# Kernel optimization log

Measured on AMD Instinct MI355X. Metric: run time of the kernel, lower is better.

Reference implementation:

```python
import jax, jax.numpy as jnp
import numpy as np

# Uniform-scope sizes: B molecules, A atoms/mol, G fragments/mol, W map width,
# H hidden, L attention layers, S = G+1 (fg prompt row prepended per molecule)
B, A, G, W, H, L = 1024, 64, 31, 8, 512, 2
S = G + 1
DK = 32  # attention head dim (hard-coded in the module)


def _layernorm(x, g, b, eps):
    mu = jnp.mean(x, axis=-1, keepdims=True)
    var = jnp.var(x, axis=-1, keepdims=True)
    return g * (x - mu) * jax.lax.rsqrt(var + eps) + b


def setup_inputs() -> dict:
    key = jax.random.key(0)
    ks = jax.random.split(key, 16)
    s = 0.02
    return {
        "f_atom": jax.random.normal(ks[0], (B * A, H), jnp.float32),
        "f_group": jax.random.normal(ks[1], (B * G, H), jnp.float32),
        "fg": jax.random.normal(ks[2], (1, 3 * H), jnp.float32),
        "alpha": 0.1 * jnp.ones((1,), jnp.float32),
        "lr_w": jax.random.normal(ks[3], (3 * H, H), jnp.float32) * s,
        "lr_b": jnp.zeros((H,), jnp.float32),
        "wq_w": jax.random.normal(ks[4], (L, H, DK), jnp.float32) * s,
        "wq_b": jnp.zeros((L, DK), jnp.float32),
        "wk_w": jax.random.normal(ks[5], (L, H, DK), jnp.float32) * s,
        "wk_b": jnp.zeros((L, DK), jnp.float32),
        "wv_w": jax.random.normal(ks[6], (L, H, DK), jnp.float32) * s,
        "wv_b": jnp.zeros((L, DK), jnp.float32),
        "dense_w": jax.random.normal(ks[7], (L, DK, H), jnp.float32) * s,
        "dense_b": jnp.zeros((L, H), jnp.float32),
        "ln_g": jnp.ones((L, H), jnp.float32),
        "ln_b": jnp.zeros((L, H), jnp.float32),
        "lin_w": jax.random.normal(ks[8], (H, H), jnp.float32) * s,
        "lin_b": jnp.zeros((H,), jnp.float32),
        "norm_g": jnp.ones((H,), jnp.float32),
        "norm_b": jnp.zeros((H,), jnp.float32),
        "mapping": jax.random.randint(ks[9], (B * G, W), 0, A + 1, jnp.int64),
    }


def reference(f_atom, f_group, fg, alpha, lr_w, lr_b, wq_w, wq_b, wk_w, wk_b,
              wv_w, wv_b, dense_w, dense_b, ln_g, ln_b, lin_w, lin_b,
              norm_g, norm_b, mapping):
    # --- ragged gather + reduce + pad (vectorized: uniform scopes) ---
    a = f_atom.reshape(B, A, H)
    # prepend zero padding row per molecule (mapping index 0 -> zeros)
    a_pad = jnp.concatenate([jnp.zeros((B, 1, H), a.dtype), a], axis=1)  # [B,A+1,H]
    m = mapping.reshape(B, G, W)
    gathered = a_pad[jnp.arange(B)[:, None, None], m]  # [B,G,W,H]
    g = f_group.reshape(B, G, H)
    cur_g = jnp.concatenate(
        [gathered.sum(axis=2), gathered.max(axis=2), g], axis=-1)  # [B,G,3H]
    brics = jnp.concatenate(
        [jnp.broadcast_to(fg[None], (B, 1, 3 * H)), cur_g], axis=1)  # [B,S,3H]

    f_frag = jax.nn.relu(brics @ lr_w + lr_b)  # [B,S,H]

    # mask built from init_hiddens = f_frag (same for every layer)
    pm = (f_frag != 0).astype(f_frag.dtype)
    mask = jnp.einsum('bsh,bth->bst', pm, pm)  # [B,S,S]
    neg = jnp.asarray(-1e9, f_frag.dtype)
    scale = 1.0 / np.sqrt(DK)

    hs = f_frag
    attn = None
    for l in range(L):
        q = hs @ wq_w[l] + wq_b[l]
        k = hs @ wk_w[l] + wk_b[l]
        v = hs @ wv_w[l] + wv_b[l]
        scores = jnp.einsum('bsd,btd->bst', q, k) * scale
        scores = jnp.where(mask == 0, neg, scores)
        attn = jax.nn.softmax(scores, axis=-1)
        x = jnp.einsum('bst,btd->bsd', attn, v)
        dh = x @ dense_w[l] + dense_b[l]  # dropout is identity in eval
        hs = _layernorm(dh + hs, ln_g[l], ln_b[l], 1e-6)

    f_out = _layernorm(hs @ lin_w + lin_b, norm_g, norm_b, 1e-5) * alpha[0]
    return f_out[:, 0, :], attn
```

## Files before the change

### kernel.cpp

```cpp
#include <hip/hip_runtime.h>

#define B_   1024
#define A_   64
#define G_   31
#define W_   8
#define H_   512
#define L_   2
#define S_   32
#define DK_  32
#define K3H_ 1536

typedef short short8 __attribute__((ext_vector_type(8)));
typedef float floatx4 __attribute__((ext_vector_type(4)));

__device__ __forceinline__ float bf2f(unsigned short u){
  union { unsigned int i; float f; } x; x.i = ((unsigned int)u) << 16; return x.f;
}
__device__ __forceinline__ unsigned short f2bf(float f){
  union { float f; unsigned int i; } x; x.f = f;
  unsigned int u = x.i;
  return (unsigned short)((u + 0x7FFFu + ((u >> 16) & 1u)) >> 16);
}
__device__ __forceinline__ void gl_lds16(const unsigned short* g, unsigned short* l){
  __builtin_amdgcn_global_load_lds((const __attribute__((address_space(1))) unsigned int*)g,
                                   (__attribute__((address_space(3))) unsigned int*)l, 16, 0, 0);
}

__global__ __launch_bounds__(256) void prep_transpose(
    const float* __restrict__ lr_w, const float* __restrict__ lin_w,
    unsigned short* __restrict__ lr_wT, unsigned short* __restrict__ lin_wT){
  __shared__ float tile[64][65];
  int bx = blockIdx.x;
  const float* src; unsigned short* dst; int R, C;
  if (bx < 192){ src = lr_w;  dst = lr_wT;  R = 1536; C = 512; }
  else         { bx -= 192; src = lin_w; dst = lin_wT; R = 512;  C = 512; }
  int rt = bx >> 3, ct = bx & 7;
  int tid = threadIdx.x;
  int r16 = tid >> 4, c4 = tid & 15;
  #pragma unroll
  for (int p = 0; p < 4; ++p){
    int row = p*16 + r16;
    float4 v = *(const float4*)(src + (size_t)(rt*64 + row) * C + ct*64 + c4*4);
    tile[row][c4*4+0] = v.x; tile[row][c4*4+1] = v.y;
    tile[row][c4*4+2] = v.z; tile[row][c4*4+3] = v.w;
  }
  __syncthreads();
  int rr = tid >> 3, cc8 = tid & 7;
  #pragma unroll
  for (int p = 0; p < 2; ++p){
    int n = p*32 + rr;
    unsigned short o[8] __attribute__((aligned(16)));
    #pragma unroll
    for (int j = 0; j < 8; ++j) o[j] = f2bf(tile[cc8*8 + j][n]);
    *(uint4*)(dst + (size_t)(ct*64 + n) * R + rt*64 + cc8*8) = *(const uint4*)o;
  }
}

__global__ __launch_bounds__(256) void prep_small(
    const float* __restrict__ wq_w, const float* __restrict__ wk_w, const float* __restrict__ wv_w,
    const float* __restrict__ dense_w,
    unsigned short* __restrict__ qkvT, unsigned short* __restrict__ denseT){
  int i = blockIdx.x * 256 + threadIdx.x;
  if (i < 98304){
    int k = i & 511; int t = i >> 9; int n = t & 31; int u = t >> 5;
    int p = u % 3, l = u / 3;
    const float* src = (p == 0) ? wq_w : (p == 1) ? wk_w : wv_w;
    qkvT[((size_t)((l*3+p)*S_ + n)) * H_ + k] = f2bf(src[((size_t)(l*H_ + k)) * DK_ + n]);
    return;
  }
  i -= 98304;
  int k = i & 31; int t = i >> 5; int n = t & 511; int l = t >> 9;
  denseT[((size_t)(l*H_ + n)) * DK_ + k] = f2bf(dense_w[((size_t)(l*DK_ + k)) * H_ + n]);
}

__global__ __launch_bounds__(256) void build_brics(
    const float* __restrict__ f_atom, const float* __restrict__ f_group,
    const float* __restrict__ fg, const int* __restrict__ mapping,
    unsigned short* __restrict__ brics){
  int pair = blockIdx.x * 4 + (threadIdx.x >> 6);
  int b = pair >> 5, s = pair & 31;
  int t = threadIdx.x & 63;
  unsigned short* out = brics + (size_t)pair * K3H_;
  if (s == 0){
    for (int k = t; k < K3H_; k += 64) out[k] = f2bf(fg[k]);
    return;
  }
  int g = s - 1;
  const int* mp = mapping + ((size_t)(b * G_ + g)) * W_;
  int c0 = t * 8;
  float sum[8], mx[8];
  #pragma unroll
  for (int j = 0; j < 8; ++j){ sum[j] = 0.f; mx[j] = -3.4e38f; }
  for (int w = 0; w < W_; ++w){
    int idx = mp[w];
    if (idx == 0){
      #pragma unroll
      for (int j = 0; j < 8; ++j) mx[j] = fmaxf(mx[j], 0.f);
    } else {
      const float* row = f_atom + ((size_t)(b * A_ + idx - 1)) * H_ + c0;
      float4 v0 = *(const float4*)row;
      float4 v1 = *(const float4*)(row + 4);
      float v[8] = {v0.x,v0.y,v0.z,v0.w,v1.x,v1.y,v1.z,v1.w};
      #pragma unroll
      for (int j = 0; j < 8; ++j){ sum[j] += v[j]; mx[j] = fmaxf(mx[j], v[j]); }
    }
  }
  const float* grow = f_group + ((size_t)(b * G_ + g)) * H_ + c0;
  float4 g0 = *(const float4*)grow;
  float4 g1 = *(const float4*)(grow + 4);
  float gv[8] = {g0.x,g0.y,g0.z,g0.w,g1.x,g1.y,g1.z,g1.w};
  unsigned short tmp[8] __attribute__((aligned(16)));
  #pragma unroll
  for (int j = 0; j < 8; ++j) tmp[j] = f2bf(sum[j]);
  *(uint4*)(out + c0) = *(const uint4*)tmp;
  #pragma unroll
  for (int j = 0; j < 8; ++j) tmp[j] = f2bf(mx[j]);
  *(uint4*)(out + 512 + c0) = *(const uint4*)tmp;
  #pragma unroll
  for (int j = 0; j < 8; ++j) tmp[j] = f2bf(gv[j]);
  *(uint4*)(out + 1024 + c0) = *(const uint4*)tmp;
}

__global__ __launch_bounds__(256) void gemm_frag(
    const unsigned short* __restrict__ brics, const unsigned short* __restrict__ wT,
    const float* __restrict__ lr_b, unsigned short* __restrict__ f_frag){
  __shared__ __align__(16) unsigned short As[128*64];
  __shared__ __align__(16) unsigned short Bs[128*64];
  int tid = threadIdx.x;
  int bx = blockIdx.x;
  int xcd = bx & 7, slot = bx >> 3;
  int mtile = xcd + 8 * (slot >> 2);
  int ntile = slot & 3;
  int rowStart = mtile * 128, colStart = ntile * 128;
  int lane = tid & 63, wave = tid >> 6;
  int m16 = lane & 15, quad = lane >> 4;
  int wm = wave >> 1, wn = wave & 1;
  floatx4 acc[4][4];
  #pragma unroll
  for (int i = 0; i < 4; ++i)
    #pragma unroll
    for (int j = 0; j < 4; ++j) acc[i][j] = (floatx4){0.f,0.f,0.f,0.f};

  int srow = tid >> 3;
  int gchunk = (tid & 7) ^ (srow & 7);
  size_t aOff[4], bOff[4];
  #pragma unroll
  for (int p = 0; p < 4; ++p){
    aOff[p] = (size_t)(rowStart + p*32 + srow) * K3H_ + gchunk*8;
    bOff[p] = (size_t)(colStart + p*32 + srow) * K3H_ + gchunk*8;
  }
  int fsw0 = ((0*4 + quad) ^ (m16 & 7)) * 8;
  int fsw1 = ((1*4 + quad) ^ (m16 & 7)) * 8;

  for (int kt = 0; kt < K3H_/64; ++kt){
    int kbase = kt * 64;
    #pragma unroll
    for (int p = 0; p < 4; ++p){
      gl_lds16(brics + aOff[p] + kbase, As + p*2048 + (size_t)tid*8);
      gl_lds16(wT    + bOff[p] + kbase, Bs + p*2048 + (size_t)tid*8);
    }
    __syncthreads();
    #pragma unroll
    for (int ks = 0; ks < 2; ++ks){
      int fsw = ks ? fsw1 : fsw0;
      short8 af[4], bfr[4];
      #pragma unroll
      for (int i = 0; i < 4; ++i){
        af[i]  = *(const short8*)(As + (wm*64 + i*16 + m16)*64 + fsw);
        bfr[i] = *(const short8*)(Bs + (wn*64 + i*16 + m16)*64 + fsw);
      }
      #pragma unroll
      for (int i = 0; i < 4; ++i)
        #pragma unroll
        for (int j = 0; j < 4; ++j)
          acc[i][j] = __builtin_amdgcn_mfma_f32_16x16x32_bf16(af[i], bfr[j], acc[i][j], 0, 0, 0);
    }
    __syncthreads();
  }
  #pragma unroll
  for (int i = 0; i < 4; ++i)
    #pragma unroll
    for (int j = 0; j < 4; ++j){
      int col = colStart + wn*64 + j*16 + m16;
      float bias = lr_b[col];
      #pragma unroll
      for (int r = 0; r < 4; ++r){
        int row = rowStart + wm*64 + i*16 + quad*4 + r;
        float v = acc[i][j][r] + bias;
        v = v > 0.f ? v : 0.f;
        f_frag[(size_t)row * H_ + col] = f2bf(v);
      }
    }
}

__global__ __launch_bounds__(256) void attn_kernel(
    const unsigned short* __restrict__ f_frag,
    const unsigned short* __restrict__ qkvT, const unsigned short* __restrict__ denseT,
    const float* __restrict__ wq_b, const float* __restrict__ wk_b, const float* __restrict__ wv_b,
    const float* __restrict__ dense_b, const float* __restrict__ ln_g, const float* __restrict__ ln_b,
    unsigned short* __restrict__ hsf, float* __restrict__ out_attn){
  const int HP = 544, TP = 40;
  __shared__ __align__(16) unsigned short hs[S_*544];
  __shared__ __align__(16) unsigned short Qs[S_*40];
  __shared__ __align__(16) unsigned short Ks[S_*40];
  __shared__ __align__(16) unsigned short Vt[S_*40];
  __shared__ __align__(16) unsigned short Ps[S_*40];
  __shared__ __align__(16) unsigned short Xs[S_*40];
  __shared__ unsigned long long pmask[S_*8];
  __shared__ unsigned int mz[S_];
  int b = blockIdx.x;
  int tid = threadIdx.x;
  int wave = tid >> 6, lane = tid & 63;
  int m16 = lane & 15, quad = lane >> 4;

  {
    int row = tid >> 3, cc = (tid & 7) * 64;
    const unsigned short* src = f_frag + ((size_t)(b * S_ + row)) * H_ + cc;
    unsigned short* dst = hs + row * HP + cc;
    #pragma unroll
    for (int k = 0; k < 64; k += 8)
      *(uint4*)(dst + k) = *(const uint4*)(src + k);
  }
  if (tid < S_) mz[tid] = 0u;
  __syncthreads();
  {
    int s = tid >> 3, w = tid & 7;
    unsigned long long m = 0ull;
    const unsigned short* hrow = hs + s * HP + w * 64;
    for (int j = 0; j < 64; ++j)
      if (hrow[j] != 0) m |= (1ull << j);
    pmask[s * 8 + w] = m;
  }
  __syncthreads();
  for (int idx = tid; idx < S_*S_; idx += 256){
    int s = idx >> 5, t2 = idx & 31;
    bool inter = false;
    #pragma unroll
    for (int w = 0; w < 8; ++w)
      inter = inter || ((pmask[s*8+w] & pmask[t2*8+w]) != 0ull);
    if (!inter) atomicOr(&mz[s], 1u << t2);
  }
  __syncthreads();

  const float scale = 0.17677669529663687f;
  for (int l = 0; l < L_; ++l){
    {
      int mt = wave >> 1, nt = wave & 1;
      floatx4 aq = {0,0,0,0}, ak = {0,0,0,0}, av = {0,0,0,0};
      const unsigned short* arow = hs + (mt*16 + m16) * HP + quad*8;
      const unsigned short* bq = qkvT + ((size_t)((l*3 + 0)*S_ + nt*16 + m16)) * H_ + quad*8;
      const unsigned short* bk = bq + (size_t)S_ * H_;
      const unsigned short* bv = bk + (size_t)S_ * H_;
      for (int k0 = 0; k0 < H_; k0 += 32){
        short8 a = *(const short8*)(arow + k0);
        aq = __builtin_amdgcn_mfma_f32_16x16x32_bf16(a, *(const short8*)(bq + k0), aq, 0,0,0);
        ak = __builtin_amdgcn_mfma_f32_16x16x32_bf16(a, *(const short8*)(bk + k0), ak, 0,0,0);
        av = __builtin_amdgcn_mfma_f32_16x16x32_bf16(a, *(const short8*)(bv + k0), av, 0,0,0);
      }
      int col = nt*16 + m16;
      float bqs = wq_b[l*DK_ + col], bks = wk_b[l*DK_ + col], bvs = wv_b[l*DK_ + col];
      #pragma unroll
      for (int r = 0; r < 4; ++r){
        int rw = mt*16 + quad*4 + r;
        Qs[rw*TP + col] = f2bf((aq[r] + bqs) * scale);
        Ks[rw*TP + col] = f2bf(ak[r] + bks);
        Vt[col*TP + rw] = f2bf(av[r] + bvs);
      }
    }
    __syncthreads();
    if (wave < 2){
      int mt = wave;
      short8 a  = *(const short8*)(Qs + (mt*16 + m16)*TP + quad*8);
      short8 b0 = *(const short8*)(Ks + m16*TP + quad*8);
      short8 b1 = *(const short8*)(Ks + (16 + m16)*TP + quad*8);
      floatx4 z = {0,0,0,0};
      floatx4 s0 = __builtin_amdgcn_mfma_f32_16x16x32_bf16(a, b0, z, 0,0,0);
      floatx4 s1 = __builtin_amdgcn_mfma_f32_16x16x32_bf16(a, b1, z, 0,0,0);
      #pragma unroll
      for (int r = 0; r < 4; ++r){
        int s = mt*16 + quad*4 + r;
        unsigned int m = mz[s];
        float v0 = ((m >> m16) & 1u) ? -1e9f : s0[r];
        float v1 = ((m >> (16 + m16)) & 1u) ? -1e9f : s1[r];
        float mx = fmaxf(v0, v1);
        #pragma unroll
        for (int d = 1; d < 16; d <<= 1) mx = fmaxf(mx, __shfl_xor(mx, d));
        float e0 = __expf(v0 - mx), e1 = __expf(v1 - mx);
        float sm = e0 + e1;
        #pragma unroll
        for (int d = 1; d < 16; d <<= 1) sm += __shfl_xor(sm, d);
        float inv = 1.f / sm;
        float p0 = e0 * inv, p1 = e1 * inv;
        Ps[s*TP + m16] = f2bf(p0);
        Ps[s*TP + 16 + m16] = f2bf(p1);
        if (l == L_ - 1){
          float* oa = out_attn + ((size_t)b * S_ + s) * S_;
          oa[m16] = p0; oa[16 + m16] = p1;
        }
      }
    }
    __syncthreads();
    {
      int mt = wave >> 1, nt = wave & 1;
      short8 a  = *(const short8*)(Ps + (mt*16 + m16)*TP + quad*8);
      short8 bv = *(const short8*)(Vt + (nt*16 + m16)*TP + quad*8);
      floatx4 z = {0,0,0,0};
      floatx4 x = __builtin_amdgcn_mfma_f32_16x16x32_bf16(a, bv, z, 0,0,0);
      #pragma unroll
      for (int r = 0; r < 4; ++r)
        Xs[(mt*16 + quad*4 + r)*TP + nt*16 + m16] = f2bf(x[r]);
    }
    __syncthreads();
    {
      short8 ax0 = *(const short8*)(Xs + m16*TP + quad*8);
      short8 ax1 = *(const short8*)(Xs + (16 + m16)*TP + quad*8);
      #pragma unroll
      for (int j = 0; j < 8; ++j){
        int col = (wave*8 + j)*16 + m16;
        short8 bw = *(const short8*)(denseT + ((size_t)(l*H_ + col)) * DK_ + quad*8);
        float db = dense_b[l*H_ + col];
        floatx4 z = {0,0,0,0};
        floatx4 d0 = __builtin_amdgcn_mfma_f32_16x16x32_bf16(ax0, bw, z, 0,0,0);
        floatx4 d1 = __builtin_amdgcn_mfma_f32_16x16x32_bf16(ax1, bw, z, 0,0,0);
        #pragma unroll
        for (int r = 0; r < 4; ++r){
          int row0 = quad*4 + r;
          float y0 = d0[r] + db + bf2f(hs[row0*HP + col]);
          hs[row0*HP + col] = f2bf(y0);
          int row1 = 16 + quad*4 + r;
          float y1 = d1[r] + db + bf2f(hs[row1*HP + col]);
          hs[row1*HP + col] = f2bf(y1);
        }
      }
    }
    __syncthreads();
    {
      #pragma unroll
      for (int rr = 0; rr < 8; ++rr){
        int row = wave*8 + rr;
        unsigned short* hrow = hs + row*HP + lane*8;
        short8 hv = *(const short8*)hrow;
        float v[8]; float s1 = 0.f, s2 = 0.f;
        #pragma unroll
        for (int j = 0; j < 8; ++j){ v[j] = bf2f((unsigned short)hv[j]); s1 += v[j]; s2 += v[j]*v[j]; }
        #pragma unroll
        for (int d = 1; d < 64; d <<= 1){ s1 += __shfl_xor(s1, d); s2 += __shfl_xor(s2, d); }
        float mean = s1 * (1.f/512.f);
        float var = s2 * (1.f/512.f) - mean*mean;
        float rs = rsqrtf(var + 1e-6f);
        unsigned short o[8] __attribute__((aligned(16)));
        #pragma unroll
        for (int j = 0; j < 8; ++j){
          int colj = lane*8 + j;
          float nv = (v[j] - mean) * rs * ln_g[l*H_ + colj] + ln_b[l*H_ + colj];
          o[j] = f2bf(nv);
        }
        *(uint4*)hrow = *(const uint4*)o;
      }
    }
    __syncthreads();
  }
  if (tid < 64){
    *(uint4*)(hsf + (size_t)b * H_ + tid*8) = *(const uint4*)(hs + tid*8);
  }
}

__global__ __launch_bounds__(256) void final_kernel(
    const unsigned short* __restrict__ hsf, const unsigned short* __restrict__ lin_wT,
    const float* __restrict__ lin_b, const float* __restrict__ norm_g, const float* __restrict__ norm_b,
    const float* __restrict__ alpha, float* __restrict__ out_f){
  const int HP = 544;
  __shared__ __align__(16) unsigned short hsb[32*544];
  int blk = blockIdx.x;
  int tid = threadIdx.x;
  int wave = tid >> 6, lane = tid & 63;
  int m16 = lane & 15, quad = lane >> 4;
  {
    int row = tid >> 3, cc = (tid & 7) * 64;
    const unsigned short* src = hsf + ((size_t)(blk*32 + row)) * H_ + cc;
    unsigned short* dst = hsb + row*HP + cc;
    #pragma unroll
    for (int k = 0; k < 64; k += 8)
      *(uint4*)(dst + k) = *(const uint4*)(src + k);
  }
  __syncthreads();
  floatx4 acc[2][8];
  #pragma unroll
  for (int mt = 0; mt < 2; ++mt)
    #pragma unroll
    for (int j = 0; j < 8; ++j) acc[mt][j] = (floatx4){0.f,0.f,0.f,0.f};
  for (int k0 = 0; k0 < H_; k0 += 32){
    short8 a0 = *(const short8*)(hsb + m16*HP + k0 + quad*8);
    short8 a1 = *(const short8*)(hsb + (16 + m16)*HP + k0 + quad*8);
    #pragma unroll
    for (int j = 0; j < 8; ++j){
      int n = (wave*8 + j)*16 + m16;
      short8 bw = *(const short8*)(lin_wT + (size_t)n * H_ + k0 + quad*8);
      acc[0][j] = __builtin_amdgcn_mfma_f32_16x16x32_bf16(a0, bw, acc[0][j], 0,0,0);
      acc[1][j] = __builtin_amdgcn_mfma_f32_16x16x32_bf16(a1, bw, acc[1][j], 0,0,0);
    }
  }
  __syncthreads();
  #pragma unroll
  for (int mt = 0; mt < 2; ++mt)
    #pragma unroll
    for (int j = 0; j < 8; ++j){
      int col = (wave*8 + j)*16 + m16;
      float lb = lin_b[col];
      #pragma unroll
      for (int r = 0; r < 4; ++r){
        int row = mt*16 + quad*4 + r;
        hsb[row*HP + col] = f2bf(acc[mt][j][r] + lb);
      }
    }
  __syncthreads();
  float al = alpha[0];
  #pragma unroll
  for (int rr = 0; rr < 8; ++rr){
    int row = wave*8 + rr;
    const unsigned short* hrow = hsb + row*HP + lane*8;
    short8 hv = *(const short8*)hrow;
    float v[8]; float s1 = 0.f, s2 = 0.f;
    #pragma unroll
    for (int j = 0; j < 8; ++j){ v[j] = bf2f((unsigned short)hv[j]); s1 += v[j]; s2 += v[j]*v[j]; }
    #pragma unroll
    for (int d = 1; d < 64; d <<= 1){ s1 += __shfl_xor(s1, d); s2 += __shfl_xor(s2, d); }
    float mean = s1 * (1.f/512.f);
    float var = s2 * (1.f/512.f) - mean*mean;
    float rs = rsqrtf(var + 1e-5f);
    float o[8];
    #pragma unroll
    for (int j = 0; j < 8; ++j){
      int colj = lane*8 + j;
      o[j] = ((v[j] - mean) * rs * norm_g[colj] + norm_b[colj]) * al;
    }
    float* op = out_f + ((size_t)(blk*32 + row)) * H_ + lane*8;
    float4 f0 = {o[0], o[1], o[2], o[3]};
    float4 f1 = {o[4], o[5], o[6], o[7]};
    *(float4*)op = f0;
    *(float4*)(op + 4) = f1;
  }
}

extern "C" void kernel_launch(void* const* d_in, const int* in_sizes, int n_in,
                              void* d_out, int out_size, void* d_ws, size_t ws_size,
                              hipStream_t stream){
  const float* f_atom  = (const float*)d_in[0];
  const float* f_group = (const float*)d_in[1];
  const float* fg      = (const float*)d_in[2];
  const float* alpha   = (const float*)d_in[3];
  const float* lr_w    = (const float*)d_in[4];
  const float* lr_b    = (const float*)d_in[5];
  const float* wq_w    = (const float*)d_in[6];
  const float* wq_b    = (const float*)d_in[7];
  const float* wk_w    = (const float*)d_in[8];
  const float* wk_b    = (const float*)d_in[9];
  const float* wv_w    = (const float*)d_in[10];
  const float* wv_b    = (const float*)d_in[11];
  const float* dense_w = (const float*)d_in[12];
  const float* dense_b = (const float*)d_in[13];
  const float* ln_g    = (const float*)d_in[14];
  const float* ln_b    = (const float*)d_in[15];
  const float* lin_w   = (const float*)d_in[16];
  const float* lin_b   = (const float*)d_in[17];
  const float* norm_g  = (const float*)d_in[18];
  const float* norm_b  = (const float*)d_in[19];
  const int*   mapping = (const int*)d_in[20];

  unsigned short* brics  = (unsigned short*)d_ws;
  unsigned short* f_frag = brics  + (size_t)32768 * 1536;
  unsigned short* lr_wT  = f_frag + (size_t)32768 * 512;
  unsigned short* qkvT   = lr_wT  + (size_t)512 * 1536;
  unsigned short* denseT = qkvT   + (size_t)2*3*32*512;
  unsigned short* lin_wT = denseT + (size_t)2*512*32;
  unsigned short* hsf    = lin_wT + (size_t)512*512;

  float* out_f    = (float*)d_out;
  float* out_attn = out_f + (size_t)B_ * H_;

  prep_transpose<<<256, 256, 0, stream>>>(lr_w, lin_w, lr_wT, lin_wT);
  prep_small<<<512, 256, 0, stream>>>(wq_w, wk_w, wv_w, dense_w, qkvT, denseT);
  build_brics<<<B_ * S_ / 4, 256, 0, stream>>>(f_atom, f_group, fg, mapping, brics);
  gemm_frag<<<(32768/128) * (512/128), 256, 0, stream>>>(brics, lr_wT, lr_b, f_frag);
  attn_kernel<<<B_, 256, 0, stream>>>(f_frag, qkvT, denseT, wq_b, wk_b, wv_b,
                                      dense_b, ln_g, ln_b, hsf, out_attn);
  final_kernel<<<B_/32, 256, 0, stream>>>(hsf, lin_wT, lin_b, norm_g, norm_b, alpha, out_f);
}
```

Baseline: 502.6 us.

## Stage per-molecule atoms in LDS for brics gather and merge weight prep kernels

build_brics now runs one block per molecule. Each block stages that molecule's 64 atom rows in shared memory, in two 256-column halves, and performs the 8-way gather-sum-max from LDS instead of issuing repeated global loads per fragment. The two weight-prep kernels are merged into one launch to save a kernel launch. The new build_brics uses 64KB of LDS per block, which limits occupancy, and the mapping load now uses int4 vectors.

```diff
diff --git a/kernel.cpp b/kernel.cpp
--- a/kernel.cpp
+++ b/kernel.cpp
@@ -21,46 +21,50 @@
   unsigned int u = x.i;
   return (unsigned short)((u + 0x7FFFu + ((u >> 16) & 1u)) >> 16);
 }
+__device__ __forceinline__ unsigned long long pack4bf(float a, float b, float c, float d){
+  return (unsigned long long)f2bf(a) | ((unsigned long long)f2bf(b) << 16)
+       | ((unsigned long long)f2bf(c) << 32) | ((unsigned long long)f2bf(d) << 48);
+}
 __device__ __forceinline__ void gl_lds16(const unsigned short* g, unsigned short* l){
   __builtin_amdgcn_global_load_lds((const __attribute__((address_space(1))) unsigned int*)g,
                                    (__attribute__((address_space(3))) unsigned int*)l, 16, 0, 0);
 }
 
-__global__ __launch_bounds__(256) void prep_transpose(
+__global__ __launch_bounds__(256) void prep_weights(
     const float* __restrict__ lr_w, const float* __restrict__ lin_w,
-    unsigned short* __restrict__ lr_wT, unsigned short* __restrict__ lin_wT){
-  __shared__ float tile[64][65];
-  int bx = blockIdx.x;
-  const float* src; unsigned short* dst; int R, C;
-  if (bx < 192){ src = lr_w;  dst = lr_wT;  R = 1536; C = 512; }
-  else         { bx -= 192; src = lin_w; dst = lin_wT; R = 512;  C = 512; }
-  int rt = bx >> 3, ct = bx & 7;
-  int tid = threadIdx.x;
-  int r16 = tid >> 4, c4 = tid & 15;
-  #pragma unroll
-  for (int p = 0; p < 4; ++p){
-    int row = p*16 + r16;
-    float4 v = *(const float4*)(src + (size_t)(rt*64 + row) * C + ct*64 + c4*4);
-    tile[row][c4*4+0] = v.x; tile[row][c4*4+1] = v.y;
-    tile[row][c4*4+2] = v.z; tile[row][c4*4+3] = v.w;
-  }
-  __syncthreads();
-  int rr = tid >> 3, cc8 = tid & 7;
-  #pragma unroll
-  for (int p = 0; p < 2; ++p){
-    int n = p*32 + rr;
-    unsigned short o[8] __attribute__((aligned(16)));
-    #pragma unroll
-    for (int j = 0; j < 8; ++j) o[j] = f2bf(tile[cc8*8 + j][n]);
-    *(uint4*)(dst + (size_t)(ct*64 + n) * R + rt*64 + cc8*8) = *(const uint4*)o;
-  }
-}
-
-__global__ __launch_bounds__(256) void prep_small(
     const float* __restrict__ wq_w, const float* __restrict__ wk_w, const float* __restrict__ wv_w,
     const float* __restrict__ dense_w,
+    unsigned short* __restrict__ lr_wT, unsigned short* __restrict__ lin_wT,
     unsigned short* __restrict__ qkvT, unsigned short* __restrict__ denseT){
-  int i = blockIdx.x * 256 + threadIdx.x;
+  int bx = blockIdx.x;
+  int tid = threadIdx.x;
+  if (bx < 256){
+    __shared__ float tile[64][65];
+    const float* src; unsigned short* dst; int R, C;
+    if (bx < 192){ src = lr_w;  dst = lr_wT;  R = 1536; C = 512; }
+    else         { bx -= 192; src = lin_w; dst = lin_wT; R = 512;  C = 512; }
+    int rt = bx >> 3, ct = bx & 7;
+    int r16 = tid >> 4, c4 = tid & 15;
+    #pragma unroll
+    for (int p = 0; p < 4; ++p){
+      int row = p*16 + r16;
+      float4 v = *(const float4*)(src + (size_t)(rt*64 + row) * C + ct*64 + c4*4);
+      tile[row][c4*4+0] = v.x; tile[row][c4*4+1] = v.y;
+      tile[row][c4*4+2] = v.z; tile[row][c4*4+3] = v.w;
+    }
+    __syncthreads();
+    int rr = tid >> 3, cc8 = tid & 7;
+    #pragma unroll
+    for (int p = 0; p < 2; ++p){
+      int n = p*32 + rr;
+      unsigned short o[8] __attribute__((aligned(16)));
+      #pragma unroll
+      for (int j = 0; j < 8; ++j) o[j] = f2bf(tile[cc8*8 + j][n]);
+      *(uint4*)(dst + (size_t)(ct*64 + n) * R + rt*64 + cc8*8) = *(const uint4*)o;
+    }
+    return;
+  }
+  int i = (bx - 256) * 256 + tid;
   if (i < 98304){
     int k = i & 511; int t = i >> 9; int n = t & 31; int u = t >> 5;
     int p = u % 3, l = u / 3;
@@ -69,56 +73,69 @@
     return;
   }
   i -= 98304;
-  int k = i & 31; int t = i >> 5; int n = t & 511; int l = t >> 9;
-  denseT[((size_t)(l*H_ + n)) * DK_ + k] = f2bf(dense_w[((size_t)(l*DK_ + k)) * H_ + n]);
+  if (i < 32768){
+    int k = i & 31; int t = i >> 5; int n = t & 511; int l = t >> 9;
+    denseT[((size_t)(l*H_ + n)) * DK_ + k] = f2bf(dense_w[((size_t)(l*DK_ + k)) * H_ + n]);
+  }
 }
 
 __global__ __launch_bounds__(256) void build_brics(
     const float* __restrict__ f_atom, const float* __restrict__ f_group,
     const float* __restrict__ fg, const int* __restrict__ mapping,
     unsigned short* __restrict__ brics){
-  int pair = blockIdx.x * 4 + (threadIdx.x >> 6);
-  int b = pair >> 5, s = pair & 31;
-  int t = threadIdx.x & 63;
-  unsigned short* out = brics + (size_t)pair * K3H_;
-  if (s == 0){
-    for (int k = t; k < K3H_; k += 64) out[k] = f2bf(fg[k]);
-    return;
-  }
-  int g = s - 1;
-  const int* mp = mapping + ((size_t)(b * G_ + g)) * W_;
-  int c0 = t * 8;
-  float sum[8], mx[8];
-  #pragma unroll
-  for (int j = 0; j < 8; ++j){ sum[j] = 0.f; mx[j] = -3.4e38f; }
-  for (int w = 0; w < W_; ++w){
-    int idx = mp[w];
-    if (idx == 0){
-      #pragma unroll
-      for (int j = 0; j < 8; ++j) mx[j] = fmaxf(mx[j], 0.f);
-    } else {
-      const float* row = f_atom + ((size_t)(b * A_ + idx - 1)) * H_ + c0;
-      float4 v0 = *(const float4*)row;
-      float4 v1 = *(const float4*)(row + 4);
-      float v[8] = {v0.x,v0.y,v0.z,v0.w,v1.x,v1.y,v1.z,v1.w};
-      #pragma unroll
-      for (int j = 0; j < 8; ++j){ sum[j] += v[j]; mx[j] = fmaxf(mx[j], v[j]); }
-    }
-  }
-  const float* grow = f_group + ((size_t)(b * G_ + g)) * H_ + c0;
-  float4 g0 = *(const float4*)grow;
-  float4 g1 = *(const float4*)(grow + 4);
-  float gv[8] = {g0.x,g0.y,g0.z,g0.w,g1.x,g1.y,g1.z,g1.w};
-  unsigned short tmp[8] __attribute__((aligned(16)));
-  #pragma unroll
-  for (int j = 0; j < 8; ++j) tmp[j] = f2bf(sum[j]);
-  *(uint4*)(out + c0) = *(const uint4*)tmp;
-  #pragma unroll
-  for (int j = 0; j < 8; ++j) tmp[j] = f2bf(mx[j]);
-  *(uint4*)(out + 512 + c0) = *(const uint4*)tmp;
-  #pragma unroll
-  for (int j = 0; j < 8; ++j) tmp[j] = f2bf(gv[j]);
-  *(uint4*)(out + 1024 + c0) = *(const uint4*)tmp;
+  __shared__ float atoms[64*256];
+  int b = blockIdx.x;
+  int tid = threadIdx.x;
+  int wave = tid >> 6, lane = tid & 63;
+  const float* fa = f_atom + (size_t)b * A_ * H_;
+  int c4 = lane * 4;
+
+  #pragma unroll
+  for (int phase = 0; phase < 2; ++phase){
+    int kb = phase * 256;
+    #pragma unroll
+    for (int j = 0; j < 16; ++j){
+      int i = j*1024 + tid*4;
+      int r = i >> 8, c = i & 255;
+      *(float4*)&atoms[i] = *(const float4*)(fa + (size_t)r*H_ + kb + c);
+    }
+    __syncthreads();
+    #pragma unroll
+    for (int q = 0; q < 8; ++q){
+      int s = wave*8 + q;
+      unsigned short* out = brics + (size_t)(b*32 + s) * K3H_;
+      if (s == 0){
+        #pragma unroll
+        for (int t3 = 0; t3 < 3; ++t3){
+          int col = t3*512 + kb + c4;
+          float4 v = *(const float4*)(fg + col);
+          *(unsigned long long*)(out + col) = pack4bf(v.x, v.y, v.z, v.w);
+        }
+      } else {
+        int g = s - 1;
+        const int* mp = mapping + ((size_t)(b * G_ + g)) * W_;
+        int4 m0 = *(const int4*)mp;
+        int4 m1 = *(const int4*)(mp + 4);
+        int id[8] = {m0.x, m0.y, m0.z, m0.w, m1.x, m1.y, m1.z, m1.w};
+        float sum[4] = {0.f, 0.f, 0.f, 0.f};
+        float mx[4]  = {-3.4e38f, -3.4e38f, -3.4e38f, -3.4e38f};
+        #pragma unroll
+        for (int w = 0; w < 8; ++w){
+          int r = id[w] > 0 ? id[w] - 1 : 0;
+          float4 v = *(const float4*)&atoms[r*256 + c4];
+          bool z = (id[w] == 0);
+          float vv[4] = {z ? 0.f : v.x, z ? 0.f : v.y, z ? 0.f : v.z, z ? 0.f : v.w};
+          #pragma unroll
+          for (int j = 0; j < 4; ++j){ sum[j] += vv[j]; mx[j] = fmaxf(mx[j], vv[j]); }
+        }
+        float4 gv = *(const float4*)(f_group + ((size_t)(b * G_ + g)) * H_ + kb + c4);
+        *(unsigned long long*)(out + kb + c4)        = pack4bf(sum[0], sum[1], sum[2], sum[3]);
+        *(unsigned long long*)(out + 512 + kb + c4)  = pack4bf(mx[0], mx[1], mx[2], mx[3]);
+        *(unsigned long long*)(out + 1024 + kb + c4) = pack4bf(gv.x, gv.y, gv.z, gv.w);
+      }
+    }
+    __syncthreads();
+  }
 }
 
 __global__ __launch_bounds__(256) void gemm_frag(
@@ -478,9 +495,9 @@
   float* out_f    = (float*)d_out;
   float* out_attn = out_f + (size_t)B_ * H_;
 
-  prep_transpose<<<256, 256, 0, stream>>>(lr_w, lin_w, lr_wT, lin_wT);
-  prep_small<<<512, 256, 0, stream>>>(wq_w, wk_w, wv_w, dense_w, qkvT, denseT);
-  build_brics<<<B_ * S_ / 4, 256, 0, stream>>>(f_atom, f_group, fg, mapping, brics);
+  prep_weights<<<768, 256, 0, stream>>>(lr_w, lin_w, wq_w, wk_w, wv_w, dense_w,
+                                        lr_wT, lin_wT, qkvT, denseT);
+  build_brics<<<B_, 256, 0, stream>>>(f_atom, f_group, fg, mapping, brics);
   gemm_frag<<<(32768/128) * (512/128), 256, 0, stream>>>(brics, lr_wT, lr_b, f_frag);
   attn_kernel<<<B_, 256, 0, stream>>>(f_frag, qkvT, denseT, wq_b, wk_b, wv_b,
                                       dense_b, ln_g, ln_b, hsf, out_attn);
```

Result: faster. 476.9 us (-5.1%).
